# Kernel tuning notes

Hardware: AMD Instinct MI355X
Metric: run time of the kernel (lower is better)

Reference implementation:

```python
import jax, jax.numpy as jnp
import numpy as np

N_EMBD = 1024
N_HEAD = 16
HEAD_DIM = N_EMBD // N_HEAD

def setup_inputs() -> dict:
    key = jax.random.key(0)
    ks = jax.random.split(key, 5)
    B, T, C = 2, 2048, N_EMBD
    s = 1.0 / np.sqrt(C)
    x = jax.random.normal(ks[0], (B, T, C), dtype=jnp.float32)
    W_qkv = jax.random.normal(ks[1], (C, 3 * C), dtype=jnp.float32) * s
    b_qkv = jax.random.normal(ks[2], (3 * C,), dtype=jnp.float32) * 0.02
    W_o = jax.random.normal(ks[3], (C, C), dtype=jnp.float32) * s
    b_o = jax.random.normal(ks[4], (C,), dtype=jnp.float32) * 0.02
    return {"x": x, "W_qkv": W_qkv, "b_qkv": b_qkv, "W_o": W_o, "b_o": b_o}

def reference(x, W_qkv, b_qkv, W_o, b_o):
    B, T, C = x.shape
    H, D = N_HEAD, HEAD_DIM
    scale = 1.0 / np.sqrt(D)
    qkv = jnp.einsum('btc,cf->btf', x, W_qkv) + b_qkv  # [B,T,3C]
    q, k, v = jnp.split(qkv, 3, axis=-1)
    # [B,H,T,D]
    q = q.reshape(B, T, H, D).transpose(0, 2, 1, 3)
    k = k.reshape(B, T, H, D).transpose(0, 2, 1, 3)
    v = v.reshape(B, T, H, D).transpose(0, 2, 1, 3)
    att = jnp.einsum('bhqd,bhkd->bhqk', q, k) * scale  # [B,H,T,T]
    causal = jnp.tril(jnp.ones((T, T), dtype=bool))
    att = jnp.where(causal[None, None], att, -jnp.inf)
    att = jax.nn.softmax(att, axis=-1)
    y = jnp.einsum('bhqk,bhkd->bhqd', att, v)  # [B,H,T,D]
    y = y.transpose(0, 2, 1, 3).reshape(B, T, C)
    return jnp.einsum('btc,cf->btf', y, W_o) + b_o
```

## Files before the change

### kernel.cpp

```cpp
#include <hip/hip_runtime.h>
#include <hip/hip_bf16.h>

#define TT 2048
#define BB 2
#define CC 1024
#define NH 16
#define HD 64

typedef __attribute__((ext_vector_type(8))) short short8;
typedef __attribute__((ext_vector_type(4))) short short4b;
typedef __attribute__((ext_vector_type(4))) float f32x4;

typedef unsigned int __attribute__((address_space(1))) ui_gas;
typedef unsigned int __attribute__((address_space(3))) ui_las;

#if __has_builtin(__builtin_amdgcn_mfma_f32_16x16x16bf16_1k)
#define PV16 1
#else
#define PV16 0
#endif

__device__ __forceinline__ float us2f(unsigned short u) {
    union { unsigned int i; float f; } v; v.i = ((unsigned int)u) << 16; return v.f;
}
__device__ __forceinline__ unsigned short f2us(float f) {
    union { float f; unsigned int i; } v; v.f = f;
    unsigned int i = v.i;
    unsigned int lsb = (i >> 16) & 1u;
    i += 0x7fffu + lsb;
    return (unsigned short)(i >> 16);
}
__device__ __forceinline__ unsigned int pack2_trunc(float a, float b) {
    union { float f; unsigned int u; } x, y; x.f = a; y.f = b;
    return (y.u & 0xffff0000u) | (x.u >> 16);
}

__device__ __forceinline__ void gl_lds16(const unsigned short* g, unsigned short* l) {
    __builtin_amdgcn_global_load_lds((const ui_gas*)g, (ui_las*)l, 16, 0, 0);
}

__global__ __launch_bounds__(64) void detect_kernel(
    const void* p0, const void* p1, const void* p2, const void* p3, const void* p4,
    int* flags)
{
    const void* ps[5] = {p0, p1, p2, p3, p4};
    const int lane = threadIdx.x;
    for (int k = 0; k < 5; ++k) {
        const unsigned short* u = (const unsigned short*)ps[k];
        int bad = 0;
        #pragma unroll
        for (int j = 0; j < 4; ++j) {
            float v = us2f(u[lane * 4 + j]);
            if (!(fabsf(v) < 1e4f)) bad = 1;
        }
        unsigned long long m = __ballot(bad != 0);
        if (lane == 0) flags[k] = (__popcll(m) < 4) ? 1 : 0;
    }
}

__device__ __forceinline__ float4 load4(const void* p, size_t i, int isbf) {
    if (isbf) {
        ushort4 u = *reinterpret_cast<const ushort4*>((const unsigned short*)p + i);
        return make_float4(us2f(u.x), us2f(u.y), us2f(u.z), us2f(u.w));
    } else {
        return *reinterpret_cast<const float4*>((const float*)p + i);
    }
}
__device__ __forceinline__ float load1(const void* p, size_t i, int isbf) {
    return isbf ? us2f(((const unsigned short*)p)[i]) : ((const float*)p)[i];
}

__global__ __launch_bounds__(256) void convert_bf16(
    const void* __restrict__ X, unsigned short* __restrict__ Y,
    const int* __restrict__ flags, int fi)
{
    const int isbf = flags[fi];
    const size_t i = ((size_t)blockIdx.x * 256 + threadIdx.x) * 8;
    float4 a = load4(X, i, isbf);
    float4 b = load4(X, i + 4, isbf);
    alignas(16) unsigned short pk[8];
    pk[0] = f2us(a.x); pk[1] = f2us(a.y); pk[2] = f2us(a.z); pk[3] = f2us(a.w);
    pk[4] = f2us(b.x); pk[5] = f2us(b.y); pk[6] = f2us(b.z); pk[7] = f2us(b.w);
    *reinterpret_cast<uint4*>(Y + i) = *reinterpret_cast<const uint4*>(pk);
}

__global__ __launch_bounds__(256) void transpose_w(
    const void* __restrict__ W, unsigned short* __restrict__ Wt,
    int Krows, int N, const int* __restrict__ flags, int fi)
{
    const int isbf = flags[fi];
    __shared__ float Ls[64 * 65];
    const int t = threadIdx.x;
    const int n0 = blockIdx.x * 64, k0 = blockIdx.y * 64;
    {
        const int r = t >> 2, cq = (t & 3) << 4;
        #pragma unroll
        for (int i = 0; i < 4; ++i) {
            float4 v = load4(W, (size_t)(k0 + r) * N + n0 + cq + i * 4, isbf);
            Ls[r * 65 + cq + i * 4 + 0] = v.x;
            Ls[r * 65 + cq + i * 4 + 1] = v.y;
            Ls[r * 65 + cq + i * 4 + 2] = v.z;
            Ls[r * 65 + cq + i * 4 + 3] = v.w;
        }
    }
    __syncthreads();
    {
        const int c = t & 63, kg = (t >> 6) * 16;
        alignas(16) unsigned short pk[16];
        #pragma unroll
        for (int i = 0; i < 16; ++i) pk[i] = f2us(Ls[(kg + i) * 65 + c]);
        unsigned short* dst = Wt + (size_t)(n0 + c) * Krows + k0 + kg;
        *reinterpret_cast<uint4*>(dst + 0) = *reinterpret_cast<const uint4*>(&pk[0]);
        *reinterpret_cast<uint4*>(dst + 8) = *reinterpret_cast<const uint4*>(&pk[8]);
    }
}

template<int WM, int WN, int NWM, int NWN>
__global__ __launch_bounds__(256) void gemm_mfma(
    const unsigned short* __restrict__ A,
    const unsigned short* __restrict__ Bt,
    const void* __restrict__ bias, void* __restrict__ C,
    int M, int N, int K,
    const int* __restrict__ flags, int biasfi, int cfi)
{
    constexpr int BM = WM * 16 * NWM, BN = WN * 16 * NWN;
    constexpr int ASL = BM / 16, BSL = BN / 16;

    const int bias_bf = (biasfi >= 0) ? flags[biasfi] : 0;
    const int c_bf    = (cfi >= 0) ? flags[cfi] : ((cfi == -2) ? 1 : 0);

    __shared__ __align__(16) unsigned short Asl[ASL * 512];
    __shared__ __align__(16) unsigned short Bsl[BSL * 512];

    const int tid = threadIdx.x;
    const int l  = tid & 63;
    const int w  = tid >> 6;
    const int wm = w / NWN, wn = w % NWN;
    const int bm = blockIdx.y * BM, bn = blockIdx.x * BN;
    const int lm = l & 15;
    const int lk = (l >> 4) * 8;

    f32x4 acc[WM][WN];
    #pragma unroll
    for (int i = 0; i < WM; ++i)
        #pragma unroll
        for (int j = 0; j < WN; ++j) acc[i][j] = (f32x4){0.f, 0.f, 0.f, 0.f};

    for (int k0 = 0; k0 < K; k0 += 32) {
        #pragma unroll
        for (int s = 0; s < ASL / 4; ++s) {
            const int r = w * (ASL / 4) + s;
            gl_lds16(A + (size_t)(bm + r * 16 + lm) * K + k0 + lk, &Asl[r * 512]);
        }
        #pragma unroll
        for (int s = 0; s < BSL / 4; ++s) {
            const int r = w * (BSL / 4) + s;
            gl_lds16(Bt + (size_t)(bn + r * 16 + lm) * K + k0 + lk, &Bsl[r * 512]);
        }
        __syncthreads();
        short8 af[WM], bf[WN];
        #pragma unroll
        for (int i = 0; i < WM; ++i)
            af[i] = *reinterpret_cast<const short8*>(&Asl[(WM * wm + i) * 512 + l * 8]);
        #pragma unroll
        for (int j = 0; j < WN; ++j)
            bf[j] = *reinterpret_cast<const short8*>(&Bsl[(WN * wn + j) * 512 + l * 8]);
        #pragma unroll
        for (int i = 0; i < WM; ++i)
            #pragma unroll
            for (int j = 0; j < WN; ++j)
                acc[i][j] = __builtin_amdgcn_mfma_f32_16x16x32_bf16(af[i], bf[j], acc[i][j], 0, 0, 0);
        __syncthreads();
    }

    const int quad = l >> 4;
    float bv[WN];
    #pragma unroll
    for (int j = 0; j < WN; ++j) bv[j] = load1(bias, bn + (WN * wn + j) * 16 + lm, bias_bf);

    #pragma unroll
    for (int i = 0; i < WM; ++i) {
        #pragma unroll
        for (int r = 0; r < 4; ++r) {
            const int row = bm + (WM * wm + i) * 16 + quad * 4 + r;
            #pragma unroll
            for (int j = 0; j < WN; ++j) {
                const int col = bn + (WN * wn + j) * 16 + lm;
                const float val = acc[i][j][r] + bv[j];
                if (c_bf) ((unsigned short*)C)[(size_t)row * N + col] = f2us(val);
                else      ((float*)C)[(size_t)row * N + col] = val;
            }
        }
    }
}

__global__ __launch_bounds__(256) void transpose_v(
    const unsigned short* __restrict__ qkv, unsigned short* __restrict__ Vt)
{
    __shared__ __align__(16) unsigned short Ls[64 * 72];
    const int tid = threadIdx.x;
    const int tt = blockIdx.x;
    const int bh = blockIdx.y;
    const int b = bh >> 4, h = bh & 15;
    {
        const int tok = tid & 63, w = tid >> 6;
        const unsigned short* src = qkv + (size_t)(b * TT + tt * 64 + tok) * 3 * CC + 2 * CC + h * HD;
        #pragma unroll
        for (int c2 = 0; c2 < 2; ++c2) {
            int c = 2 * w + c2;
            uint4 d = *(const uint4*)(src + c * 8);
            *(uint4*)(&Ls[tok * 72 + c * 8]) = d;
        }
    }
    __syncthreads();
    {
        const int d = tid >> 2, kq = tid & 3;
        unsigned short out[16];
        #pragma unroll
        for (int i = 0; i < 16; ++i) out[i] = Ls[(kq * 16 + i) * 72 + d];
        unsigned short* dst = Vt + (size_t)bh * HD * TT + (size_t)d * TT + tt * 64 + kq * 16;
        *(uint4*)(dst + 0) = *(uint4*)(&out[0]);
        *(uint4*)(dst + 8) = *(uint4*)(&out[8]);
    }
}

__global__ __launch_bounds__(256) void attn_mfma(
    const unsigned short* __restrict__ qkv,
    const unsigned short* __restrict__ Vt,
    unsigned short* __restrict__ y)
{
    __shared__ __align__(16) unsigned short Ksh[8 * 512];
#if PV16
    __shared__ __align__(16) unsigned short Vsh[1039 * 4];
#else
    __shared__ __align__(16) unsigned short Vsh[1039 * 8];
#endif

    const int tid = threadIdx.x;
    const int l   = tid & 63;
    const int w   = tid >> 6;
    const int quad = l >> 4;
    const int col  = l & 15;

    const int n  = blockIdx.x;
    const int bh = (n & 7) * 4 + ((n >> 3) & 3);
    const int qt = 31 - (n >> 5);
    const int b  = bh >> 4, h = bh & 15;

#if !PV16
    for (int s = tid; s < 1039; s += 256)
        *(uint2*)(&Vsh[s * 8 + 4]) = make_uint2(0u, 0u);
#endif

    const float QSCALE = 0.18033688f;
    short8 qf[2];
    {
        const int token = qt * 64 + w * 16 + col;
        const unsigned short* qrow = qkv + (size_t)(b * TT + token) * 3 * CC + h * HD;
        #pragma unroll
        for (int ks = 0; ks < 2; ++ks) {
            ushort4 u0 = *(const ushort4*)(qrow + ks * 32 + quad * 8);
            ushort4 u1 = *(const ushort4*)(qrow + ks * 32 + quad * 8 + 4);
            alignas(16) unsigned short pk[8];
            pk[0] = f2us(us2f(u0.x) * QSCALE);
            pk[1] = f2us(us2f(u0.y) * QSCALE);
            pk[2] = f2us(us2f(u0.z) * QSCALE);
            pk[3] = f2us(us2f(u0.w) * QSCALE);
            pk[4] = f2us(us2f(u1.x) * QSCALE);
            pk[5] = f2us(us2f(u1.y) * QSCALE);
            pk[6] = f2us(us2f(u1.z) * QSCALE);
            pk[7] = f2us(us2f(u1.w) * QSCALE);
            qf[ks] = *(const short8*)pk;
        }
    }

    f32x4 o[4];
    #pragma unroll
    for (int nb = 0; nb < 4; ++nb) o[nb] = (f32x4){0.f, 0.f, 0.f, 0.f};
    float m_i = -3e38f, l_i = 0.f;

    const unsigned short* kbase = qkv + (size_t)b * TT * 3 * CC + CC + h * HD;
    const unsigned short* vbase = Vt + (size_t)bh * HD * TT;

    const int vd = tid >> 2, vg0 = (tid & 3) * 4;

    uint4 rk[2], rv[2];
    auto issue_loads = [&](int kt) {
        const unsigned short* ksrc = kbase + (size_t)(kt * 64 + l) * 3 * CC;
        #pragma unroll
        for (int c2 = 0; c2 < 2; ++c2) {
            const int c = 2 * w + c2;
            rk[c2] = *(const uint4*)(ksrc + c * 8);
        }
        const unsigned short* vsrc = vbase + (size_t)vd * TT + kt * 64 + vg0 * 4;
        rv[0] = *(const uint4*)(vsrc + 0);
        rv[1] = *(const uint4*)(vsrc + 8);
    };
    auto write_lds = [&]() {
        #pragma unroll
        for (int c2 = 0; c2 < 2; ++c2) {
            const int c = 2 * w + c2;
            const int ks = c >> 2, q = c & 3;
            const int slot = ((quad * 2 + ks) * 64 + q * 16 + col) * 8;
            *(uint4*)(&Ksh[slot]) = rk[c2];
        }
#if PV16
        *(uint2*)(&Vsh[((vg0 + 0) * 65 + vd) * 4]) = make_uint2(rv[0].x, rv[0].y);
        *(uint2*)(&Vsh[((vg0 + 1) * 65 + vd) * 4]) = make_uint2(rv[0].z, rv[0].w);
        *(uint2*)(&Vsh[((vg0 + 2) * 65 + vd) * 4]) = make_uint2(rv[1].x, rv[1].y);
        *(uint2*)(&Vsh[((vg0 + 3) * 65 + vd) * 4]) = make_uint2(rv[1].z, rv[1].w);
#else
        *(uint2*)(&Vsh[((vg0 + 0) * 65 + vd) * 8]) = make_uint2(rv[0].x, rv[0].y);
        *(uint2*)(&Vsh[((vg0 + 1) * 65 + vd) * 8]) = make_uint2(rv[0].z, rv[0].w);
        *(uint2*)(&Vsh[((vg0 + 2) * 65 + vd) * 8]) = make_uint2(rv[1].x, rv[1].y);
        *(uint2*)(&Vsh[((vg0 + 3) * 65 + vd) * 8]) = make_uint2(rv[1].z, rv[1].w);
#endif
    };

    auto step = [&](bool diag) {
        f32x4 st[4];
        #pragma unroll
        for (int nb = 0; nb < 4; ++nb) {
            f32x4 acc = {0.f, 0.f, 0.f, 0.f};
            #pragma unroll
            for (int ks = 0; ks < 2; ++ks) {
                short8 kf = *(const short8*)(&Ksh[((nb * 2 + ks) * 64 + l) * 8]);
                acc = __builtin_amdgcn_mfma_f32_16x16x32_bf16(kf, qf[ks], acc, 0, 0, 0);
            }
            st[nb] = acc;
        }
        float sv[4][4];
        #pragma unroll
        for (int nb = 0; nb < 4; ++nb)
            #pragma unroll
            for (int r = 0; r < 4; ++r) {
                float v = st[nb][r];
                if (diag && (nb * 16 + quad * 4 + r > w * 16 + col)) v = -3e38f;
                sv[nb][r] = v;
            }
        float rm = sv[0][0];
        #pragma unroll
        for (int nb = 0; nb < 4; ++nb)
            #pragma unroll
            for (int r = 0; r < 4; ++r) rm = fmaxf(rm, sv[nb][r]);
        rm = fmaxf(rm, __shfl_xor(rm, 16));
        rm = fmaxf(rm, __shfl_xor(rm, 32));
        const float mn = fmaxf(m_i, rm);
        const float al = __builtin_exp2f(m_i - mn);
        float pv[4][4];
        float rs = 0.f;
        #pragma unroll
        for (int nb = 0; nb < 4; ++nb)
            #pragma unroll
            for (int r = 0; r < 4; ++r) {
                float p = __builtin_exp2f(sv[nb][r] - mn);
                pv[nb][r] = p;
                rs += p;
            }
        rs += __shfl_xor(rs, 16);
        rs += __shfl_xor(rs, 32);
        l_i = l_i * al + rs;
        m_i = mn;
        float alr[4];
        #pragma unroll
        for (int r = 0; r < 4; ++r) alr[r] = __shfl(al, quad * 4 + r);
        #pragma unroll
        for (int nb = 0; nb < 4; ++nb)
            #pragma unroll
            for (int r = 0; r < 4; ++r) o[nb][r] *= alr[r];
#if PV16
        short4b pf[4];
        #pragma unroll
        for (int nbk = 0; nbk < 4; ++nbk) {
            union { short4b s; unsigned int u[2]; } pk;
            pk.u[0] = pack2_trunc(pv[nbk][0], pv[nbk][1]);
            pk.u[1] = pack2_trunc(pv[nbk][2], pv[nbk][3]);
            pf[nbk] = pk.s;
        }
        #pragma unroll
        for (int nbd = 0; nbd < 4; ++nbd)
            #pragma unroll
            for (int nbk = 0; nbk < 4; ++nbk) {
                short4b vf = *(const short4b*)(&Vsh[((nbk * 4 + quad) * 65 + nbd * 16 + col) * 4]);
                o[nbd] = __builtin_amdgcn_mfma_f32_16x16x16bf16_1k(pf[nbk], vf, o[nbd], 0, 0, 0);
            }
#else
        short8 pf[4];
        #pragma unroll
        for (int nbk = 0; nbk < 4; ++nbk) {
            union { short8 s; unsigned int u[4]; } pk;
            pk.u[0] = pack2_trunc(pv[nbk][0], pv[nbk][1]);
            pk.u[1] = pack2_trunc(pv[nbk][2], pv[nbk][3]);
            pk.u[2] = 0u; pk.u[3] = 0u;
            pf[nbk] = pk.s;
        }
        #pragma unroll
        for (int nbd = 0; nbd < 4; ++nbd)
            #pragma unroll
            for (int nbk = 0; nbk < 4; ++nbk) {
                short8 vf = *(const short8*)(&Vsh[((nbk * 4 + quad) * 65 + nbd * 16 + col) * 8]);
                o[nbd] = __builtin_amdgcn_mfma_f32_16x16x32_bf16(pf[nbk], vf, o[nbd], 0, 0, 0);
            }
#endif
    };

    issue_loads(0);
    for (int kt = 0; kt <= qt; ++kt) {
        write_lds();
        __syncthreads();
        if (kt < qt) issue_loads(kt + 1);
        step(kt == qt);
        __syncthreads();
    }

    {
        const float inv = 1.f / l_i;
        float invr[4];
        #pragma unroll
        for (int r = 0; r < 4; ++r) invr[r] = __shfl(inv, quad * 4 + r);
        #pragma unroll
        for (int nb = 0; nb < 4; ++nb)
            #pragma unroll
            for (int r = 0; r < 4; ++r) {
                int token = qt * 64 + w * 16 + quad * 4 + r;
                y[(size_t)(b * TT + token) * CC + h * HD + nb * 16 + col] = f2us(o[nb][r] * invr[r]);
            }
    }
}

extern "C" void kernel_launch(void* const* d_in, const int* in_sizes, int n_in,
                              void* d_out, int out_size, void* d_ws, size_t ws_size,
                              hipStream_t stream) {
    const int M = BB * TT;

    char* ws = (char*)d_ws;
    int*            flags = (int*)ws;                         ws += 256;
    unsigned short* xb    = (unsigned short*)ws;              ws += (size_t)M * CC * 2;
    unsigned short* Wqkvt = (unsigned short*)ws;              ws += (size_t)3 * CC * CC * 2;
    unsigned short* Wot   = (unsigned short*)ws;              ws += (size_t)CC * CC * 2;
    unsigned short* qkv   = (unsigned short*)ws;              ws += (size_t)M * 3 * CC * 2;
    unsigned short* Vt    = (unsigned short*)ws;              ws += (size_t)BB * NH * HD * TT * 2;
    unsigned short* y     = (unsigned short*)ws;

    detect_kernel<<<1, 64, 0, stream>>>(d_in[0], d_in[1], d_in[2], d_in[3], d_in[4], flags);

    convert_bf16<<<(M * CC) / (256 * 8), 256, 0, stream>>>(d_in[0], xb, flags, 0);
    transpose_w<<<dim3(3 * CC / 64, CC / 64), 256, 0, stream>>>(d_in[1], Wqkvt, CC, 3 * CC, flags, 1);
    transpose_w<<<dim3(CC / 64, CC / 64), 256, 0, stream>>>(d_in[3], Wot, CC, CC, flags, 3);

    gemm_mfma<4, 4, 2, 2><<<dim3(3 * CC / 128, M / 128), 256, 0, stream>>>(
        xb, Wqkvt, d_in[2], qkv, M, 3 * CC, CC, flags, 2, -2);

    transpose_v<<<dim3(TT / 64, BB * NH), 256, 0, stream>>>(qkv, Vt);

    attn_mfma<<<1024, 256, 0, stream>>>(qkv, Vt, y);

    gemm_mfma<2, 4, 4, 1><<<dim3(CC / 64, M / 128), 256, 0, stream>>>(
        y, Wot, d_in[4], d_out, M, CC, CC, flags, 4, 0);
}
```

Before: 252.9 us.

## Pair causal query tiles per attention block and merge prep kernels

```diff
diff --git a/kernel.cpp b/kernel.cpp
--- a/kernel.cpp
+++ b/kernel.cpp
@@ -70,33 +70,56 @@
     return isbf ? us2f(((const unsigned short*)p)[i]) : ((const float*)p)[i];
 }
 
-__global__ __launch_bounds__(256) void convert_bf16(
-    const void* __restrict__ X, unsigned short* __restrict__ Y,
-    const int* __restrict__ flags, int fi)
+__global__ __launch_bounds__(256) void prep_kernel(
+    const void* __restrict__ x, const void* __restrict__ Wqkv, const void* __restrict__ Wo,
+    unsigned short* __restrict__ xb, unsigned short* __restrict__ Wqkvt,
+    unsigned short* __restrict__ Wot)
 {
-    const int isbf = flags[fi];
-    const size_t i = ((size_t)blockIdx.x * 256 + threadIdx.x) * 8;
-    float4 a = load4(X, i, isbf);
-    float4 b = load4(X, i + 4, isbf);
-    alignas(16) unsigned short pk[8];
-    pk[0] = f2us(a.x); pk[1] = f2us(a.y); pk[2] = f2us(a.z); pk[3] = f2us(a.w);
-    pk[4] = f2us(b.x); pk[5] = f2us(b.y); pk[6] = f2us(b.z); pk[7] = f2us(b.w);
-    *reinterpret_cast<uint4*>(Y + i) = *reinterpret_cast<const uint4*>(pk);
-}
-
-__global__ __launch_bounds__(256) void transpose_w(
-    const void* __restrict__ W, unsigned short* __restrict__ Wt,
-    int Krows, int N, const int* __restrict__ flags, int fi)
-{
-    const int isbf = flags[fi];
     __shared__ float Ls[64 * 65];
+    __shared__ int sh_isbf;
     const int t = threadIdx.x;
-    const int n0 = blockIdx.x * 64, k0 = blockIdx.y * 64;
+    const int bid = blockIdx.x;
+
+    const void* src;
+    int mode, sub;
+    if (bid < 2048)      { mode = 0; sub = bid;        src = x; }
+    else if (bid < 2816) { mode = 1; sub = bid - 2048; src = Wqkv; }
+    else                 { mode = 2; sub = bid - 2816; src = Wo; }
+
+    if (t < 64) {
+        const unsigned short* u = (const unsigned short*)src;
+        int bad = 0;
+        #pragma unroll
+        for (int j = 0; j < 4; ++j) {
+            float v = us2f(u[t * 4 + j]);
+            if (!(fabsf(v) < 1e4f)) bad = 1;
+        }
+        unsigned long long m = __ballot(bad != 0);
+        if (t == 0) sh_isbf = (__popcll(m) < 4) ? 1 : 0;
+    }
+    __syncthreads();
+    const int isbf = sh_isbf;
+
+    if (mode == 0) {
+        const size_t i = ((size_t)sub * 256 + t) * 8;
+        float4 a = load4(src, i, isbf);
+        float4 b = load4(src, i + 4, isbf);
+        alignas(16) unsigned short pk[8];
+        pk[0] = f2us(a.x); pk[1] = f2us(a.y); pk[2] = f2us(a.z); pk[3] = f2us(a.w);
+        pk[4] = f2us(b.x); pk[5] = f2us(b.y); pk[6] = f2us(b.z); pk[7] = f2us(b.w);
+        *reinterpret_cast<uint4*>(xb + i) = *reinterpret_cast<const uint4*>(pk);
+        return;
+    }
+
+    int N, Krows, n0, k0;
+    unsigned short* dst;
+    if (mode == 1) { N = 3 * CC; Krows = CC; dst = Wqkvt; n0 = (sub % 48) * 64; k0 = (sub / 48) * 64; }
+    else           { N = CC;     Krows = CC; dst = Wot;   n0 = (sub % 16) * 64; k0 = (sub / 16) * 64; }
     {
         const int r = t >> 2, cq = (t & 3) << 4;
         #pragma unroll
         for (int i = 0; i < 4; ++i) {
-            float4 v = load4(W, (size_t)(k0 + r) * N + n0 + cq + i * 4, isbf);
+            float4 v = load4(src, (size_t)(k0 + r) * N + n0 + cq + i * 4, isbf);
             Ls[r * 65 + cq + i * 4 + 0] = v.x;
             Ls[r * 65 + cq + i * 4 + 1] = v.y;
             Ls[r * 65 + cq + i * 4 + 2] = v.z;
@@ -109,9 +132,9 @@
         alignas(16) unsigned short pk[16];
         #pragma unroll
         for (int i = 0; i < 16; ++i) pk[i] = f2us(Ls[(kg + i) * 65 + c]);
-        unsigned short* dst = Wt + (size_t)(n0 + c) * Krows + k0 + kg;
-        *reinterpret_cast<uint4*>(dst + 0) = *reinterpret_cast<const uint4*>(&pk[0]);
-        *reinterpret_cast<uint4*>(dst + 8) = *reinterpret_cast<const uint4*>(&pk[8]);
+        unsigned short* d = dst + (size_t)(n0 + c) * Krows + k0 + kg;
+        *reinterpret_cast<uint4*>(d + 0) = *reinterpret_cast<const uint4*>(&pk[0]);
+        *reinterpret_cast<uint4*>(d + 8) = *reinterpret_cast<const uint4*>(&pk[8]);
     }
 }
 
@@ -230,11 +253,7 @@
     unsigned short* __restrict__ y)
 {
     __shared__ __align__(16) unsigned short Ksh[8 * 512];
-#if PV16
-    __shared__ __align__(16) unsigned short Vsh[1039 * 4];
-#else
     __shared__ __align__(16) unsigned short Vsh[1039 * 8];
-#endif
 
     const int tid = threadIdx.x;
     const int l   = tid & 63;
@@ -243,18 +262,21 @@
     const int col  = l & 15;
 
     const int n  = blockIdx.x;
-    const int bh = (n & 7) * 4 + ((n >> 3) & 3);
-    const int qt = 31 - (n >> 5);
+    const int g  = n >> 3;
+    const int bh = (n & 7) * 4 + (g & 3);
+    const int i  = g >> 2;
+    const int tA = i, tB = 31 - i;
     const int b  = bh >> 4, h = bh & 15;
 
-#if !PV16
     for (int s = tid; s < 1039; s += 256)
         *(uint2*)(&Vsh[s * 8 + 4]) = make_uint2(0u, 0u);
-#endif
 
     const float QSCALE = 0.18033688f;
-    short8 qf[2];
-    {
+    short8 qfA[2], qfB[2];
+    #pragma unroll
+    for (int t2 = 0; t2 < 2; ++t2) {
+        const int qt = t2 ? tB : tA;
+        short8* qf = t2 ? qfB : qfA;
         const int token = qt * 64 + w * 16 + col;
         const unsigned short* qrow = qkv + (size_t)(b * TT + token) * 3 * CC + h * HD;
         #pragma unroll
@@ -274,10 +296,13 @@
         }
     }
 
-    f32x4 o[4];
-    #pragma unroll
-    for (int nb = 0; nb < 4; ++nb) o[nb] = (f32x4){0.f, 0.f, 0.f, 0.f};
-    float m_i = -3e38f, l_i = 0.f;
+    f32x4 oA[4], oB[4];
+    #pragma unroll
+    for (int nb = 0; nb < 4; ++nb) {
+        oA[nb] = (f32x4){0.f, 0.f, 0.f, 0.f};
+        oB[nb] = (f32x4){0.f, 0.f, 0.f, 0.f};
+    }
+    float mA = -3e38f, lAc = 0.f, mB = -3e38f, lBc = 0.f;
 
     const unsigned short* kbase = qkv + (size_t)b * TT * 3 * CC + CC + h * HD;
     const unsigned short* vbase = Vt + (size_t)bh * HD * TT;
@@ -304,20 +329,13 @@
             const int slot = ((quad * 2 + ks) * 64 + q * 16 + col) * 8;
             *(uint4*)(&Ksh[slot]) = rk[c2];
         }
-#if PV16
-        *(uint2*)(&Vsh[((vg0 + 0) * 65 + vd) * 4]) = make_uint2(rv[0].x, rv[0].y);
-        *(uint2*)(&Vsh[((vg0 + 1) * 65 + vd) * 4]) = make_uint2(rv[0].z, rv[0].w);
-        *(uint2*)(&Vsh[((vg0 + 2) * 65 + vd) * 4]) = make_uint2(rv[1].x, rv[1].y);
-        *(uint2*)(&Vsh[((vg0 + 3) * 65 + vd) * 4]) = make_uint2(rv[1].z, rv[1].w);
-#else
         *(uint2*)(&Vsh[((vg0 + 0) * 65 + vd) * 8]) = make_uint2(rv[0].x, rv[0].y);
         *(uint2*)(&Vsh[((vg0 + 1) * 65 + vd) * 8]) = make_uint2(rv[0].z, rv[0].w);
         *(uint2*)(&Vsh[((vg0 + 2) * 65 + vd) * 8]) = make_uint2(rv[1].x, rv[1].y);
         *(uint2*)(&Vsh[((vg0 + 3) * 65 + vd) * 8]) = make_uint2(rv[1].z, rv[1].w);
-#endif
     };
 
-    auto step = [&](bool diag) {
+    auto step = [&](const short8* qf, f32x4* o, float& m_i, float& l_i, bool diag) {
         f32x4 st[4];
         #pragma unroll
         for (int nb = 0; nb < 4; ++nb) {
@@ -346,7 +364,6 @@
         rm = fmaxf(rm, __shfl_xor(rm, 16));
         rm = fmaxf(rm, __shfl_xor(rm, 32));
         const float mn = fmaxf(m_i, rm);
-        const float al = __builtin_exp2f(m_i - mn);
         float pv[4][4];
         float rs = 0.f;
         #pragma unroll
@@ -359,15 +376,20 @@
             }
         rs += __shfl_xor(rs, 16);
         rs += __shfl_xor(rs, 32);
-        l_i = l_i * al + rs;
+        if (__ballot(mn > m_i) != 0ull) {
+            const float al = __builtin_exp2f(m_i - mn);
+            l_i = l_i * al + rs;
+            float alr[4];
+            #pragma unroll
+            for (int r = 0; r < 4; ++r) alr[r] = __shfl(al, quad * 4 + r);
+            #pragma unroll
+            for (int nb = 0; nb < 4; ++nb)
+                #pragma unroll
+                for (int r = 0; r < 4; ++r) o[nb][r] *= alr[r];
+        } else {
+            l_i += rs;
+        }
         m_i = mn;
-        float alr[4];
-        #pragma unroll
-        for (int r = 0; r < 4; ++r) alr[r] = __shfl(al, quad * 4 + r);
-        #pragma unroll
-        for (int nb = 0; nb < 4; ++nb)
-            #pragma unroll
-            for (int r = 0; r < 4; ++r) o[nb][r] *= alr[r];
 #if PV16
         short4b pf[4];
         #pragma unroll
@@ -381,7 +403,7 @@
         for (int nbd = 0; nbd < 4; ++nbd)
             #pragma unroll
             for (int nbk = 0; nbk < 4; ++nbk) {
-                short4b vf = *(const short4b*)(&Vsh[((nbk * 4 + quad) * 65 + nbd * 16 + col) * 4]);
+                short4b vf = *(const short4b*)(&Vsh[((nbk * 4 + quad) * 65 + nbd * 16 + col) * 8]);
                 o[nbd] = __builtin_amdgcn_mfma_f32_16x16x16bf16_1k(pf[nbk], vf, o[nbd], 0, 0, 0);
             }
 #else
@@ -405,16 +427,20 @@
     };
 
     issue_loads(0);
-    for (int kt = 0; kt <= qt; ++kt) {
+    for (int kt = 0; kt <= tB; ++kt) {
         write_lds();
         __syncthreads();
-        if (kt < qt) issue_loads(kt + 1);
-        step(kt == qt);
+        if (kt < tB) issue_loads(kt + 1);
+        step(qfB, oB, mB, lBc, kt == tB);
+        if (kt <= tA) step(qfA, oA, mA, lAc, kt == tA);
         __syncthreads();
     }
 
-    {
-        const float inv = 1.f / l_i;
+    #pragma unroll
+    for (int t2 = 0; t2 < 2; ++t2) {
+        const int qt = t2 ? tB : tA;
+        f32x4* o = t2 ? oB : oA;
+        const float inv = 1.f / (t2 ? lBc : lAc);
         float invr[4];
         #pragma unroll
         for (int r = 0; r < 4; ++r) invr[r] = __shfl(inv, quad * 4 + r);
@@ -444,16 +470,14 @@
 
     detect_kernel<<<1, 64, 0, stream>>>(d_in[0], d_in[1], d_in[2], d_in[3], d_in[4], flags);
 
-    convert_bf16<<<(M * CC) / (256 * 8), 256, 0, stream>>>(d_in[0], xb, flags, 0);
-    transpose_w<<<dim3(3 * CC / 64, CC / 64), 256, 0, stream>>>(d_in[1], Wqkvt, CC, 3 * CC, flags, 1);
-    transpose_w<<<dim3(CC / 64, CC / 64), 256, 0, stream>>>(d_in[3], Wot, CC, CC, flags, 3);
+    prep_kernel<<<3072, 256, 0, stream>>>(d_in[0], d_in[1], d_in[3], xb, Wqkvt, Wot);
 
     gemm_mfma<4, 4, 2, 2><<<dim3(3 * CC / 128, M / 128), 256, 0, stream>>>(
         xb, Wqkvt, d_in[2], qkv, M, 3 * CC, CC, flags, 2, -2);
 
     transpose_v<<<dim3(TT / 64, BB * NH), 256, 0, stream>>>(qkv, Vt);
 
-    attn_mfma<<<1024, 256, 0, stream>>>(qkv, Vt, y);
+    attn_mfma<<<512, 256, 0, stream>>>(qkv, Vt, y);
 
     gemm_mfma<2, 4, 4, 1><<<dim3(CC / 64, M / 128), 256, 0, stream>>>(
         y, Wot, d_in[4], d_out, M, CC, CC, flags, 4, 0);
```

Result: faster. 239.0 us (-5.5%).
